# Performance work log

Hardware: AMD Instinct MI355X
Metric: run time of the kernel (lower is better)

The kernel has to match this reference:

```python
import jax, jax.numpy as jnp
import numpy as np

BINS = 256

def setup_inputs() -> dict:
    key = jax.random.key(0)
    x = jax.random.normal(key, (64, 3, 512, 512), dtype=jnp.float32)
    return {"x": x}

def reference(x):
    bins = BINS

    def equalize_one(img):
        # img: (C, H, W) -- flattened wholesale, matching the torch per-index loop
        flat = img.reshape(-1)
        mn = flat.min()
        mx = flat.max()
        norm = (flat - mn) * (bins - 1) / (mx - mn + 1e-8)
        norm = jnp.clip(norm, 0, bins - 1)
        idx = norm.astype(jnp.int32)  # bucket index per pixel
        hist = jnp.zeros((bins,), jnp.float32).at[idx].add(1.0)  # bincount
        cdf = jnp.cumsum(hist)
        cdf_norm = (cdf - cdf.min()) / (cdf.max() - cdf.min() + 1e-8)
        return cdf_norm[idx].reshape(img.shape)  # gather equalized values

    return jax.vmap(equalize_one)(x)
```

## Files before the change

kernel.cpp:

```cpp
#include <hip/hip_runtime.h>

#define NUM_BINS 256
#define NPI (3*512*512)
#define TPB 256
#define MMX_BLOCKS 32
#define MM_BLOCKS 16
#define GB_PER_IMG 32
#define NSUB 32
#define SUBSTRIDE 257
#define G_VEC 8

typedef float f32x4 __attribute__((ext_vector_type(4)));

__device__ __forceinline__ int bin_of(float v, float mn, float denom) {
  float norm = (v - mn) * 255.0f / denom;
  norm = fminf(fmaxf(norm, 0.0f), 255.0f);
  return (int)norm;
}

__device__ __forceinline__ unsigned pack4(int b0, int b1, int b2, int b3) {
  return (unsigned)b0 | ((unsigned)b1 << 8) | ((unsigned)b2 << 16) | ((unsigned)b3 << 24);
}

__global__ void minmax_k(const float4* __restrict__ x,
                         float* __restrict__ mmn, float* __restrict__ mmx) {
  const int chunk4 = NPI / 4 / MMX_BLOCKS;
  int img = blockIdx.x / MMX_BLOCKS;
  int blk = blockIdx.x % MMX_BLOCKS;
  const float4* p = x + (size_t)img * (NPI/4) + (size_t)blk * chunk4;
  float mn = 3.4e38f, mx = -3.4e38f;
  #pragma unroll 4
  for (int i = threadIdx.x; i < chunk4; i += TPB) {
    float4 v = p[i];
    mn = fminf(mn, fminf(fminf(v.x, v.y), fminf(v.z, v.w)));
    mx = fmaxf(mx, fmaxf(fmaxf(v.x, v.y), fmaxf(v.z, v.w)));
  }
  for (int off = 32; off > 0; off >>= 1) {
    mn = fminf(mn, __shfl_down(mn, off));
    mx = fmaxf(mx, __shfl_down(mx, off));
  }
  __shared__ float smn[4], smx[4];
  int wave = threadIdx.x >> 6, lane = threadIdx.x & 63;
  if (lane == 0) { smn[wave] = mn; smx[wave] = mx; }
  __syncthreads();
  if (threadIdx.x == 0) {
    mmn[blockIdx.x] = fminf(fminf(smn[0], smn[1]), fminf(smn[2], smn[3]));
    mmx[blockIdx.x] = fmaxf(fmaxf(smx[0], smx[1]), fmaxf(smx[2], smx[3]));
  }
}

__device__ __forceinline__ void load_minmax(const float* __restrict__ mmn,
                                            const float* __restrict__ mmx,
                                            int img, float* s_mn, float* s_dn) {
  if (threadIdx.x < MMX_BLOCKS) {
    float a = mmn[img * MMX_BLOCKS + threadIdx.x];
    float b = mmx[img * MMX_BLOCKS + threadIdx.x];
    for (int off = MMX_BLOCKS / 2; off > 0; off >>= 1) {
      a = fminf(a, __shfl_down(a, off));
      b = fmaxf(b, __shfl_down(b, off));
    }
    if (threadIdx.x == 0) { *s_mn = a; *s_dn = b - a + 1e-8f; }
  }
}

__global__ void hist_k(const float4* __restrict__ x,
                       const float* __restrict__ mmn, const float* __restrict__ mmx,
                       int* __restrict__ histblk, unsigned* __restrict__ bins32) {
  __shared__ int sh[NSUB * SUBSTRIDE];
  __shared__ float s_mn, s_dn;
  load_minmax(mmn, mmx, blockIdx.x / MM_BLOCKS, &s_mn, &s_dn);
  for (int i = threadIdx.x; i < NSUB * SUBSTRIDE; i += TPB) sh[i] = 0;
  const int chunk4 = NPI / 4 / MM_BLOCKS;
  int img = blockIdx.x / MM_BLOCKS;
  int blk = blockIdx.x % MM_BLOCKS;
  __syncthreads();
  float mn = s_mn, denom = s_dn;
  size_t gbase = (size_t)img * (NPI/4) + (size_t)blk * chunk4;
  const float4* p = x + gbase;
  int* mysub = sh + (threadIdx.x & (NSUB - 1)) * SUBSTRIDE;
  bool wb = (bins32 != nullptr);
  for (int i = threadIdx.x; i < chunk4; i += TPB * 8) {
    float4 v[8];
    #pragma unroll
    for (int k = 0; k < 8; ++k) v[k] = p[i + k * TPB];
    int b[8][4];
    #pragma unroll
    for (int k = 0; k < 8; ++k) {
      b[k][0] = bin_of(v[k].x, mn, denom);
      b[k][1] = bin_of(v[k].y, mn, denom);
      b[k][2] = bin_of(v[k].z, mn, denom);
      b[k][3] = bin_of(v[k].w, mn, denom);
    }
    #pragma unroll
    for (int k = 0; k < 8; ++k) {
      atomicAdd(&mysub[b[k][0]], 1);
      atomicAdd(&mysub[b[k][1]], 1);
      atomicAdd(&mysub[b[k][2]], 1);
      atomicAdd(&mysub[b[k][3]], 1);
    }
    if (wb) {
      #pragma unroll
      for (int k = 0; k < 8; ++k)
        bins32[gbase + i + k * TPB] = pack4(b[k][0], b[k][1], b[k][2], b[k][3]);
    }
  }
  __syncthreads();
  int bin = threadIdx.x;
  int s = 0;
  #pragma unroll
  for (int c = 0; c < NSUB; ++c) s += sh[c * SUBSTRIDE + bin];
  histblk[blockIdx.x * NUM_BINS + bin] = s;
}

__global__ void gather_bins_k(const unsigned* __restrict__ bins32,
                              const int* __restrict__ histblk,
                              float4* __restrict__ out) {
  __shared__ int s[NUM_BINS];
  __shared__ float c[NUM_BINS];
  const int f4pi = NPI / 4;
  const int chunk4 = f4pi / GB_PER_IMG;
  const int ITERS = chunk4 / (TPB * G_VEC);
  int img = blockIdx.x / GB_PER_IMG;
  int blk = blockIdx.x % GB_PER_IMG;
  int t = threadIdx.x;
  int v = 0;
  #pragma unroll
  for (int b = 0; b < MM_BLOCKS; ++b)
    v += histblk[(img * MM_BLOCKS + b) * NUM_BINS + t];
  s[t] = v;
  __syncthreads();
  for (int off = 1; off < NUM_BINS; off <<= 1) {
    int add = (t >= off) ? s[t - off] : 0;
    __syncthreads();
    s[t] += add;
    __syncthreads();
  }
  {
    int cdf = s[t], c0 = s[0], cN = s[NUM_BINS - 1];
    c[t] = (float)(cdf - c0) / ((float)(cN - c0) + 1e-8f);
  }
  __syncthreads();
  size_t base = (size_t)img * f4pi + (size_t)blk * chunk4 + threadIdx.x;
  for (int it = 0; it < ITERS; ++it) {
    size_t b0 = base + (size_t)it * TPB * G_VEC;
    unsigned bv[G_VEC];
    #pragma unroll
    for (int j = 0; j < G_VEC; ++j) bv[j] = bins32[b0 + (size_t)j * TPB];
    #pragma unroll
    for (int j = 0; j < G_VEC; ++j) {
      unsigned b = bv[j];
      f32x4 o;
      o.x = c[b & 255u];
      o.y = c[(b >> 8) & 255u];
      o.z = c[(b >> 16) & 255u];
      o.w = c[b >> 24];
      __builtin_nontemporal_store(o, (f32x4*)&out[b0 + (size_t)j * TPB]);
    }
  }
}

__global__ void scan_k(const int* __restrict__ histblk, float* __restrict__ cdfn) {
  __shared__ int s[NUM_BINS];
  int img = blockIdx.x, t = threadIdx.x;
  int v = 0;
  #pragma unroll
  for (int b = 0; b < MM_BLOCKS; ++b)
    v += histblk[(img * MM_BLOCKS + b) * NUM_BINS + t];
  s[t] = v;
  __syncthreads();
  for (int off = 1; off < NUM_BINS; off <<= 1) {
    int add = (t >= off) ? s[t - off] : 0;
    __syncthreads();
    s[t] += add;
    __syncthreads();
  }
  int cdf = s[t], c0 = s[0], cN = s[NUM_BINS - 1];
  cdfn[img * NUM_BINS + t] = (float)(cdf - c0) / ((float)(cN - c0) + 1e-8f);
}

__global__ void gather_x_k(const float4* __restrict__ x,
                           const float* __restrict__ mmn, const float* __restrict__ mmx,
                           const float* __restrict__ cdfn,
                           float4* __restrict__ out) {
  __shared__ float c[NUM_BINS];
  __shared__ float s_mn, s_dn;
  const int f4pi = NPI / 4;
  const int CHUNK = TPB * 4;
  const int bpi = f4pi / CHUNK;
  int img = blockIdx.x / bpi;
  int blk = blockIdx.x % bpi;
  c[threadIdx.x] = cdfn[img * NUM_BINS + threadIdx.x];
  load_minmax(mmn, mmx, img, &s_mn, &s_dn);
  __syncthreads();
  float mn = s_mn, denom = s_dn;
  size_t base = (size_t)img * f4pi + (size_t)blk * CHUNK + threadIdx.x;
  #pragma unroll
  for (int j = 0; j < 4; ++j) {
    float4 v = x[base + (size_t)j * TPB];
    f32x4 o;
    o.x = c[bin_of(v.x, mn, denom)];
    o.y = c[bin_of(v.y, mn, denom)];
    o.z = c[bin_of(v.z, mn, denom)];
    o.w = c[bin_of(v.w, mn, denom)];
    __builtin_nontemporal_store(o, (f32x4*)&out[base + (size_t)j * TPB]);
  }
}

extern "C" void kernel_launch(void* const* d_in, const int* in_sizes, int n_in,
                              void* d_out, int out_size, void* d_ws, size_t ws_size,
                              hipStream_t stream) {
  const float* x = (const float*)d_in[0];
  float* out = (float*)d_out;
  int B = in_sizes[0] / NPI;

  char* ws = (char*)d_ws;
  float* mmn = (float*)ws;
  float* mmx = mmn + (size_t)B * MMX_BLOCKS;
  int* histblk = (int*)(mmx + (size_t)B * MMX_BLOCKS);
  float* cdfn = (float*)(histblk + (size_t)B * MM_BLOCKS * NUM_BINS);
  unsigned* bins32 = (unsigned*)(cdfn + (size_t)B * NUM_BINS);
  size_t need = (size_t)((char*)bins32 - ws) + (size_t)B * NPI;
  bool use_bins = (ws_size >= need);

  minmax_k<<<B * MMX_BLOCKS, TPB, 0, stream>>>((const float4*)x, mmn, mmx);
  hist_k<<<B * MM_BLOCKS, TPB, 0, stream>>>((const float4*)x, mmn, mmx, histblk,
                                            use_bins ? bins32 : nullptr);
  if (use_bins) {
    gather_bins_k<<<B * GB_PER_IMG, TPB, 0, stream>>>(bins32, histblk, (float4*)out);
  } else {
    scan_k<<<B, NUM_BINS, 0, stream>>>(histblk, cdfn);
    gather_x_k<<<B * (NPI/4/(TPB*4)), TPB, 0, stream>>>((const float4*)x, mmn, mmx, cdfn,
                                                        (float4*)out);
  }
}
```

Baseline: 376.0 us.

## Split histogram pass into separate binize and packed-bin histogram kernels

The fused hist kernel, which read floats, computed bins, did LDS atomics and wrote packed bins, becomes two kernels. binize_k streams x to packed uint8 bins at full bandwidth, and histb_k rebuilds the histogram from the 4x smaller bins buffer. The idea is to decouple the latency-bound atomic phase from the bandwidth-bound float read. This costs an extra launch and an extra read of the bins buffer (about a quarter of the input size). The minmax loop is also fully unrolled with four loads in flight.

```diff
diff --git a/kernel.cpp b/kernel.cpp
--- a/kernel.cpp
+++ b/kernel.cpp
@@ -4,6 +4,7 @@
 #define NPI (3*512*512)
 #define TPB 256
 #define MMX_BLOCKS 32
+#define BZ_BLOCKS 32
 #define MM_BLOCKS 16
 #define GB_PER_IMG 32
 #define NSUB 32
@@ -29,11 +30,21 @@
   int blk = blockIdx.x % MMX_BLOCKS;
   const float4* p = x + (size_t)img * (NPI/4) + (size_t)blk * chunk4;
   float mn = 3.4e38f, mx = -3.4e38f;
-  #pragma unroll 4
-  for (int i = threadIdx.x; i < chunk4; i += TPB) {
-    float4 v = p[i];
-    mn = fminf(mn, fminf(fminf(v.x, v.y), fminf(v.z, v.w)));
-    mx = fmaxf(mx, fmaxf(fmaxf(v.x, v.y), fmaxf(v.z, v.w)));
+  #pragma unroll
+  for (int it = 0; it < chunk4 / (TPB * 4); ++it) {
+    int i0 = threadIdx.x + it * TPB * 4;
+    float4 v0 = p[i0];
+    float4 v1 = p[i0 + TPB];
+    float4 v2 = p[i0 + 2*TPB];
+    float4 v3 = p[i0 + 3*TPB];
+    mn = fminf(mn, fminf(fminf(v0.x, v0.y), fminf(v0.z, v0.w)));
+    mx = fmaxf(mx, fmaxf(fmaxf(v0.x, v0.y), fmaxf(v0.z, v0.w)));
+    mn = fminf(mn, fminf(fminf(v1.x, v1.y), fminf(v1.z, v1.w)));
+    mx = fmaxf(mx, fmaxf(fmaxf(v1.x, v1.y), fmaxf(v1.z, v1.w)));
+    mn = fminf(mn, fminf(fminf(v2.x, v2.y), fminf(v2.z, v2.w)));
+    mx = fmaxf(mx, fmaxf(fmaxf(v2.x, v2.y), fmaxf(v2.z, v2.w)));
+    mn = fminf(mn, fminf(fminf(v3.x, v3.y), fminf(v3.z, v3.w)));
+    mx = fmaxf(mx, fmaxf(fmaxf(v3.x, v3.y), fmaxf(v3.z, v3.w)));
   }
   for (int off = 32; off > 0; off >>= 1) {
     mn = fminf(mn, __shfl_down(mn, off));
@@ -63,45 +74,57 @@
   }
 }
 
-__global__ void hist_k(const float4* __restrict__ x,
-                       const float* __restrict__ mmn, const float* __restrict__ mmx,
-                       int* __restrict__ histblk, unsigned* __restrict__ bins32) {
+__global__ void binize_k(const float4* __restrict__ x,
+                         const float* __restrict__ mmn, const float* __restrict__ mmx,
+                         unsigned* __restrict__ bins32) {
+  __shared__ float s_mn, s_dn;
+  load_minmax(mmn, mmx, blockIdx.x / BZ_BLOCKS, &s_mn, &s_dn);
+  __syncthreads();
+  float mn = s_mn, denom = s_dn;
+  const int chunk4 = NPI / 4 / BZ_BLOCKS;
+  int img = blockIdx.x / BZ_BLOCKS;
+  int blk = blockIdx.x % BZ_BLOCKS;
+  size_t gbase = (size_t)img * (NPI/4) + (size_t)blk * chunk4;
+  const float4* p = x + gbase;
+  unsigned* q = bins32 + gbase;
+  #pragma unroll
+  for (int it = 0; it < chunk4 / (TPB * 4); ++it) {
+    int i0 = threadIdx.x + it * TPB * 4;
+    float4 v0 = p[i0];
+    float4 v1 = p[i0 + TPB];
+    float4 v2 = p[i0 + 2*TPB];
+    float4 v3 = p[i0 + 3*TPB];
+    q[i0]         = pack4(bin_of(v0.x, mn, denom), bin_of(v0.y, mn, denom),
+                          bin_of(v0.z, mn, denom), bin_of(v0.w, mn, denom));
+    q[i0 + TPB]   = pack4(bin_of(v1.x, mn, denom), bin_of(v1.y, mn, denom),
+                          bin_of(v1.z, mn, denom), bin_of(v1.w, mn, denom));
+    q[i0 + 2*TPB] = pack4(bin_of(v2.x, mn, denom), bin_of(v2.y, mn, denom),
+                          bin_of(v2.z, mn, denom), bin_of(v2.w, mn, denom));
+    q[i0 + 3*TPB] = pack4(bin_of(v3.x, mn, denom), bin_of(v3.y, mn, denom),
+                          bin_of(v3.z, mn, denom), bin_of(v3.w, mn, denom));
+  }
+}
+
+__global__ void histb_k(const unsigned* __restrict__ bins32,
+                        int* __restrict__ histblk) {
   __shared__ int sh[NSUB * SUBSTRIDE];
-  __shared__ float s_mn, s_dn;
-  load_minmax(mmn, mmx, blockIdx.x / MM_BLOCKS, &s_mn, &s_dn);
   for (int i = threadIdx.x; i < NSUB * SUBSTRIDE; i += TPB) sh[i] = 0;
-  const int chunk4 = NPI / 4 / MM_BLOCKS;
+  __syncthreads();
+  const int wpb = NPI / 4 / MM_BLOCKS;
   int img = blockIdx.x / MM_BLOCKS;
   int blk = blockIdx.x % MM_BLOCKS;
-  __syncthreads();
-  float mn = s_mn, denom = s_dn;
-  size_t gbase = (size_t)img * (NPI/4) + (size_t)blk * chunk4;
-  const float4* p = x + gbase;
+  const unsigned* p = bins32 + (size_t)img * (NPI/4) + (size_t)blk * wpb;
   int* mysub = sh + (threadIdx.x & (NSUB - 1)) * SUBSTRIDE;
-  bool wb = (bins32 != nullptr);
-  for (int i = threadIdx.x; i < chunk4; i += TPB * 8) {
-    float4 v[8];
+  for (int it = 0; it < wpb / (TPB * 8); ++it) {
+    unsigned w[8];
     #pragma unroll
-    for (int k = 0; k < 8; ++k) v[k] = p[i + k * TPB];
-    int b[8][4];
+    for (int k = 0; k < 8; ++k) w[k] = p[threadIdx.x + it * TPB * 8 + k * TPB];
     #pragma unroll
     for (int k = 0; k < 8; ++k) {
-      b[k][0] = bin_of(v[k].x, mn, denom);
-      b[k][1] = bin_of(v[k].y, mn, denom);
-      b[k][2] = bin_of(v[k].z, mn, denom);
-      b[k][3] = bin_of(v[k].w, mn, denom);
-    }
-    #pragma unroll
-    for (int k = 0; k < 8; ++k) {
-      atomicAdd(&mysub[b[k][0]], 1);
-      atomicAdd(&mysub[b[k][1]], 1);
-      atomicAdd(&mysub[b[k][2]], 1);
-      atomicAdd(&mysub[b[k][3]], 1);
-    }
-    if (wb) {
-      #pragma unroll
-      for (int k = 0; k < 8; ++k)
-        bins32[gbase + i + k * TPB] = pack4(b[k][0], b[k][1], b[k][2], b[k][3]);
+      atomicAdd(&mysub[w[k] & 255u], 1);
+      atomicAdd(&mysub[(w[k] >> 8) & 255u], 1);
+      atomicAdd(&mysub[(w[k] >> 16) & 255u], 1);
+      atomicAdd(&mysub[w[k] >> 24], 1);
     }
   }
   __syncthreads();
@@ -159,6 +182,50 @@
   }
 }
 
+__global__ void hist_k(const float4* __restrict__ x,
+                       const float* __restrict__ mmn, const float* __restrict__ mmx,
+                       int* __restrict__ histblk) {
+  __shared__ int sh[NSUB * SUBSTRIDE];
+  __shared__ float s_mn, s_dn;
+  load_minmax(mmn, mmx, blockIdx.x / MM_BLOCKS, &s_mn, &s_dn);
+  for (int i = threadIdx.x; i < NSUB * SUBSTRIDE; i += TPB) sh[i] = 0;
+  const int chunk4 = NPI / 4 / MM_BLOCKS;
+  int img = blockIdx.x / MM_BLOCKS;
+  int blk = blockIdx.x % MM_BLOCKS;
+  __syncthreads();
+  float mn = s_mn, denom = s_dn;
+  const float4* p = x + (size_t)img * (NPI/4) + (size_t)blk * chunk4;
+  int* mysub = sh + (threadIdx.x & (NSUB - 1)) * SUBSTRIDE;
+  for (int i = threadIdx.x; i < chunk4; i += TPB * 4) {
+    float4 v0 = p[i];
+    float4 v1 = p[i + TPB];
+    float4 v2 = p[i + 2*TPB];
+    float4 v3 = p[i + 3*TPB];
+    atomicAdd(&mysub[bin_of(v0.x, mn, denom)], 1);
+    atomicAdd(&mysub[bin_of(v0.y, mn, denom)], 1);
+    atomicAdd(&mysub[bin_of(v0.z, mn, denom)], 1);
+    atomicAdd(&mysub[bin_of(v0.w, mn, denom)], 1);
+    atomicAdd(&mysub[bin_of(v1.x, mn, denom)], 1);
+    atomicAdd(&mysub[bin_of(v1.y, mn, denom)], 1);
+    atomicAdd(&mysub[bin_of(v1.z, mn, denom)], 1);
+    atomicAdd(&mysub[bin_of(v1.w, mn, denom)], 1);
+    atomicAdd(&mysub[bin_of(v2.x, mn, denom)], 1);
+    atomicAdd(&mysub[bin_of(v2.y, mn, denom)], 1);
+    atomicAdd(&mysub[bin_of(v2.z, mn, denom)], 1);
+    atomicAdd(&mysub[bin_of(v2.w, mn, denom)], 1);
+    atomicAdd(&mysub[bin_of(v3.x, mn, denom)], 1);
+    atomicAdd(&mysub[bin_of(v3.y, mn, denom)], 1);
+    atomicAdd(&mysub[bin_of(v3.z, mn, denom)], 1);
+    atomicAdd(&mysub[bin_of(v3.w, mn, denom)], 1);
+  }
+  __syncthreads();
+  int bin = threadIdx.x;
+  int s = 0;
+  #pragma unroll
+  for (int c = 0; c < NSUB; ++c) s += sh[c * SUBSTRIDE + bin];
+  histblk[blockIdx.x * NUM_BINS + bin] = s;
+}
+
 __global__ void scan_k(const int* __restrict__ histblk, float* __restrict__ cdfn) {
   __shared__ int s[NUM_BINS];
   int img = blockIdx.x, t = threadIdx.x;
@@ -223,11 +290,12 @@
   bool use_bins = (ws_size >= need);
 
   minmax_k<<<B * MMX_BLOCKS, TPB, 0, stream>>>((const float4*)x, mmn, mmx);
-  hist_k<<<B * MM_BLOCKS, TPB, 0, stream>>>((const float4*)x, mmn, mmx, histblk,
-                                            use_bins ? bins32 : nullptr);
   if (use_bins) {
+    binize_k<<<B * BZ_BLOCKS, TPB, 0, stream>>>((const float4*)x, mmn, mmx, bins32);
+    histb_k<<<B * MM_BLOCKS, TPB, 0, stream>>>(bins32, histblk);
     gather_bins_k<<<B * GB_PER_IMG, TPB, 0, stream>>>(bins32, histblk, (float4*)out);
   } else {
+    hist_k<<<B * MM_BLOCKS, TPB, 0, stream>>>((const float4*)x, mmn, mmx, histblk);
     scan_k<<<B, NUM_BINS, 0, stream>>>(histblk, cdfn);
     gather_x_k<<<B * (NPI/4/(TPB*4)), TPB, 0, stream>>>((const float4*)x, mmn, mmx, cdfn,
                                                         (float4*)out);
```

Measured after the change: 384.9 us. 2.4% more time.
